# Kernel optimization log

Hardware: AMD Instinct MI355X
Metric: run time of the kernel (lower is better)

The kernel has to match this reference:

```python
import jax, jax.numpy as jnp
import numpy as np

N_NODES = 50000
N_EDGES = 800000
IN_CH, HID, OUT_CH = 3, 64, 768
NEG_SLOPE = 0.01  # torch LeakyReLU default
BN_EPS = 1e-5


def _gcn_conv(x, edge_index, W, b):
    # PyG GCNConv: add self-loops, symmetric degree normalization, scatter-add.
    n = x.shape[0]
    loops = jnp.arange(n, dtype=edge_index.dtype)
    src = jnp.concatenate([edge_index[0], loops])
    dst = jnp.concatenate([edge_index[1], loops])
    deg = jax.ops.segment_sum(jnp.ones(src.shape[0], x.dtype), dst, num_segments=n)
    dinv = jnp.where(deg > 0, jax.lax.rsqrt(deg), 0.0)
    norm = dinv[src] * dinv[dst]                      # [E+N]
    h = x @ W                                          # [N, out]
    msg = h[src] * norm[:, None]                       # gather + edge scale
    return jax.ops.segment_sum(msg, dst, num_segments=n) + b


def _block(x, edge_index, W, b, gamma, beta):
    h = _gcn_conv(x, edge_index, W, b)
    h = jnp.where(h >= 0, h, NEG_SLOPE * h)            # LeakyReLU
    mean = h.mean(axis=0)
    var = h.var(axis=0)                                # biased, as torch BN train
    h = (h - mean) * jax.lax.rsqrt(var + BN_EPS) * gamma + beta
    return h                                           # dropout: identity (eval)


def _glorot(key, fan_in, fan_out):
    s = np.sqrt(6.0 / (fan_in + fan_out)).astype(np.float32)
    return jax.random.uniform(key, (fan_in, fan_out), jnp.float32, -s, s)


def setup_inputs() -> dict:
    key = jax.random.key(0)
    ks = jax.random.split(key, 8)
    x = jax.random.normal(ks[0], (N_NODES, IN_CH), jnp.float32)
    edge_index = jax.random.randint(ks[1], (2, N_EDGES), 0, N_NODES, jnp.int64)
    inp = {"x": x, "edge_index": edge_index}
    inp["W1"] = _glorot(ks[2], IN_CH, HID)
    inp["b1"] = jnp.zeros((HID,), jnp.float32)
    inp["g1"] = jnp.ones((HID,), jnp.float32)
    inp["be1"] = jnp.zeros((HID,), jnp.float32)
    inp["W2"] = _glorot(ks[3], HID, HID)
    inp["b2"] = jnp.zeros((HID,), jnp.float32)
    inp["g2"] = jnp.ones((HID,), jnp.float32)
    inp["be2"] = jnp.zeros((HID,), jnp.float32)
    inp["W3"] = _glorot(ks[4], HID, HID)
    inp["b3"] = jnp.zeros((HID,), jnp.float32)
    inp["g3"] = jnp.ones((HID,), jnp.float32)
    inp["be3"] = jnp.zeros((HID,), jnp.float32)
    inp["Wmu"] = _glorot(ks[5], HID, OUT_CH)
    inp["bmu"] = jnp.zeros((OUT_CH,), jnp.float32)
    inp["Wls"] = _glorot(ks[6], HID, OUT_CH)
    inp["bls"] = jnp.zeros((OUT_CH,), jnp.float32)
    return inp


def reference(x, edge_index, W1, b1, g1, be1, W2, b2, g2, be2, W3, b3, g3, be3, Wmu, bmu, Wls, bls):
    h = _block(x, edge_index, W1, b1, g1, be1)
    h = _block(h, edge_index, W2, b2, g2, be2)
    h = _block(h, edge_index, W3, b3, g3, be3)
    mu = _gcn_conv(h, edge_index, Wmu, bmu)
    logstd = _gcn_conv(h, edge_index, Wls, bls)
    return (mu, logstd)
```

## Files before the change

kernel.cpp:

```cpp
#include <hip/hip_runtime.h>
#include <cstddef>


#define NEG_SLOPE 0.01f
#define BN_EPS 1e-5f

__global__ __launch_bounds__(256) void init_k(int* __restrict__ cnt,
                                              float* __restrict__ bns, int N) {
  int i = blockIdx.x * 256 + threadIdx.x;
  if (i < N) cnt[i] = 0;
  if (i < 384) bns[i] = 0.0f;
}

__global__ __launch_bounds__(256) void hist_k(const int* __restrict__ dst,
                                              int* __restrict__ cnt, int E) {
  int e = blockIdx.x * 256 + threadIdx.x;
  if (e < E) atomicAdd(&cnt[dst[e]], 1);
}

__global__ __launch_bounds__(1024) void scanA(const int* __restrict__ cnt,
                                              int* __restrict__ pre,
                                              int* __restrict__ bsum, int N) {
  __shared__ int sh[1024];
  const int t = threadIdx.x;
  const int i = blockIdx.x * 1024 + t;
  int c = (i < N) ? cnt[i] : 0;
  sh[t] = c;
  __syncthreads();
  for (int off = 1; off < 1024; off <<= 1) {
    int v = (t >= off) ? sh[t - off] : 0;
    __syncthreads();
    sh[t] += v;
    __syncthreads();
  }
  if (i < N) pre[i] = sh[t] - c;
  if (t == 1023) bsum[blockIdx.x] = sh[t];
}

__global__ __launch_bounds__(64) void scanB(int* __restrict__ bsum, int nb) {
  int t = threadIdx.x;
  int orig = (t < nb) ? bsum[t] : 0;
  int v = orig;
#pragma unroll
  for (int off = 1; off < 64; off <<= 1) {
    int u = __shfl_up(v, off);
    if (t >= off) v += u;
  }
  if (t < nb) bsum[t] = v - orig;
}

__global__ __launch_bounds__(256) void scanC(const int* __restrict__ cnt,
                                             int* __restrict__ rowptr,
                                             int* __restrict__ cursor,
                                             const int* __restrict__ bsum,
                                             float* __restrict__ dinv,
                                             int N, int E) {
  int i = blockIdx.x * 256 + threadIdx.x;
  if (i < N) {
    int rp = rowptr[i] + bsum[i >> 10];
    rowptr[i] = rp;
    cursor[i] = rp;
    dinv[i] = rsqrtf((float)(cnt[i] + 1));
  }
  if (i == 0) rowptr[N] = E;
}

__global__ __launch_bounds__(256) void fill_k(const int* __restrict__ src,
                                              const int* __restrict__ dst,
                                              int* __restrict__ cursor,
                                              int* __restrict__ eidx, int E) {
  int e = blockIdx.x * 256 + threadIdx.x;
  if (e >= E) return;
  int p = atomicAdd(&cursor[dst[e]], 1);
  eidx[p] = src[e];
}

__global__ __launch_bounds__(256) void l1_fused(
    const int* __restrict__ rowptr, const int* __restrict__ eidx,
    const float* __restrict__ x, const float* __restrict__ dinv,
    const float* __restrict__ W1, const float* __restrict__ b1,
    float* __restrict__ Z, float* __restrict__ q, float* __restrict__ bns, int N) {
  const int t = threadIdx.x, lane = t & 63, wid = t >> 6;
  const int gw = blockIdx.x * 4 + wid;
  const int nw = gridDim.x * 4;
  const float w0 = W1[lane], w1 = W1[64 + lane], w2 = W1[128 + lane];
  const float bb = b1[lane];
  float s1 = 0.f, s2 = 0.f;
  for (int node = gw; node < N; node += nw) {
    int beg = rowptr[node], end = rowptr[node + 1];
    float a0 = 0.f, a1 = 0.f, a2 = 0.f, aq = 0.f;
    for (int e = beg + lane; e < end; e += 64) {
      int s = eidx[e];
      float dv = dinv[s];
      a0 += x[s * 3] * dv;
      a1 += x[s * 3 + 1] * dv;
      a2 += x[s * 3 + 2] * dv;
      aq += dv;
    }
#pragma unroll
    for (int off = 32; off; off >>= 1) {
      a0 += __shfl_xor(a0, off);
      a1 += __shfl_xor(a1, off);
      a2 += __shfl_xor(a2, off);
      aq += __shfl_xor(aq, off);
    }
    float dv = dinv[node];
    a0 += x[node * 3] * dv;
    a1 += x[node * 3 + 1] * dv;
    a2 += x[node * 3 + 2] * dv;
    aq += dv;
    float u = dv * (a0 * w0 + a1 * w1 + a2 * w2) + bb;
    float o = u >= 0.f ? u : NEG_SLOPE * u;
    Z[(size_t)node * 64 + lane] = o * dv;
    s1 += o;
    s2 += o * o;
    if (lane == 0) q[node] = aq;
  }
  __shared__ float red[8][64];
  red[wid][lane] = s1;
  red[4 + wid][lane] = s2;
  __syncthreads();
  if (t < 64) {
    atomicAdd(&bns[t], red[0][t] + red[1][t] + red[2][t] + red[3][t]);
    atomicAdd(&bns[64 + t], red[4][t] + red[5][t] + red[6][t] + red[7][t]);
  }
}

__global__ __launch_bounds__(256) void gather64(const int* __restrict__ rowptr,
                                                const int* __restrict__ eidx,
                                                const float* __restrict__ Z,
                                                float* __restrict__ G, int N) {
  int node = blockIdx.x * 4 + (threadIdx.x >> 6);
  if (node >= N) return;
  int lane = threadIdx.x & 63;
  int slot = lane >> 4;
  int c4 = (lane & 15) << 2;
  int beg = rowptr[node], end = rowptr[node + 1];
  float ax = 0.f, ay = 0.f, az = 0.f, aw = 0.f;
  int e = beg + slot;
  for (; e + 4 < end; e += 8) {
    int s0 = eidx[e], s1 = eidx[e + 4];
    float4 v0 = *(const float4*)(Z + (size_t)s0 * 64 + c4);
    float4 v1 = *(const float4*)(Z + (size_t)s1 * 64 + c4);
    ax += v0.x + v1.x;
    ay += v0.y + v1.y;
    az += v0.z + v1.z;
    aw += v0.w + v1.w;
  }
  if (e < end) {
    int s0 = eidx[e];
    float4 v0 = *(const float4*)(Z + (size_t)s0 * 64 + c4);
    ax += v0.x; ay += v0.y; az += v0.z; aw += v0.w;
  }
#pragma unroll
  for (int off = 16; off < 64; off <<= 1) {
    ax += __shfl_xor(ax, off);
    ay += __shfl_xor(ay, off);
    az += __shfl_xor(az, off);
    aw += __shfl_xor(aw, off);
  }
  if (slot == 0) {
    float4 self = *(const float4*)(Z + (size_t)node * 64 + c4);
    float4 o = make_float4(ax + self.x, ay + self.y, az + self.z, aw + self.w);
    *(float4*)(G + (size_t)node * 64 + c4) = o;
  }
}

__global__ __launch_bounds__(256) void prep_small(
    const float* __restrict__ bns, const float* __restrict__ g,
    const float* __restrict__ be, const float* __restrict__ W,
    float* __restrict__ Wc, float* __restrict__ cx, float invN) {
  __shared__ float sc[64], sh[64], part[4][64];
  int t = threadIdx.x;
  if (t < 64) {
    float mean = bns[t] * invN;
    float var = bns[64 + t] * invN - mean * mean;
    float s = g[t] * rsqrtf(var + BN_EPS);
    sc[t] = s;
    sh[t] = be[t] - mean * s;
  }
  __syncthreads();
  int c = t & 63, kq = t >> 6;
  float p = 0.f;
  for (int k = kq * 16; k < kq * 16 + 16; ++k) {
    float w = W[k * 64 + c];
    Wc[k * 64 + c] = sc[k] * w;
    p += sh[k] * w;
  }
  part[kq][c] = p;
  __syncthreads();
  if (t < 64) cx[t] = part[0][t] + part[1][t] + part[2][t] + part[3][t];
}

__global__ __launch_bounds__(256) void prep_head(
    const float* __restrict__ bns, const float* __restrict__ g,
    const float* __restrict__ be, const float* __restrict__ Wmu,
    const float* __restrict__ Wls, float* __restrict__ Wmc,
    float* __restrict__ Wlc, float* __restrict__ cmu, float* __restrict__ cls,
    float invN) {
  __shared__ float sc[64], sh[64], part[2][128];
  int t = threadIdx.x;
  if (t < 64) {
    float mean = bns[t] * invN;
    float var = bns[64 + t] * invN - mean * mean;
    float s = g[t] * rsqrtf(var + BN_EPS);
    sc[t] = s;
    sh[t] = be[t] - mean * s;
  }
  __syncthreads();
  int blk = blockIdx.x;
  int head = blk >= 6 ? 1 : 0;
  int c0 = (head ? blk - 6 : blk) * 128;
  const float* W = head ? Wls : Wmu;
  float* Wc = head ? Wlc : Wmc;
  float* cx = head ? cls : cmu;
  int c = c0 + (t & 127), kh = t >> 7;
  float p = 0.f;
  for (int k = kh * 32; k < kh * 32 + 32; ++k) {
    float w = W[(size_t)k * 768 + c];
    Wc[(size_t)k * 768 + c] = sc[k] * w;
    p += sh[k] * w;
  }
  part[kh][t & 127] = p;
  __syncthreads();
  if (t < 128) cx[c0 + t] = part[0][t] + part[1][t];
}

__global__ __launch_bounds__(256, 4) void gemm_bnq(
    const float* __restrict__ G, const float* __restrict__ dinv,
    const float* __restrict__ q, const float* __restrict__ Wc,
    const float* __restrict__ cx, const float* __restrict__ b,
    float* __restrict__ Z, float* __restrict__ bns, int N) {
  __shared__ __align__(16) float P[64][68];
  __shared__ __align__(16) float Ws[64][64];
  const int t = threadIdx.x;
  const int r0 = blockIdx.x * 64;

  for (int i = t; i < 1024; i += 256) {
    int r = i >> 4, k4 = (i & 15) << 2, gr = r0 + r;
    float4 v = make_float4(0.f, 0.f, 0.f, 0.f);
    if (gr < N) v = *(const float4*)(G + (size_t)gr * 64 + k4);
    *(float4*)&P[r][k4] = v;
  }
  for (int i = t; i < 4096; i += 256) Ws[i >> 6][i & 63] = Wc[i];
  __syncthreads();

  const int tr = t >> 4, tc4 = (t & 15) << 2;
  float acc[4][4] = {};
#pragma unroll 8
  for (int k = 0; k < 64; ++k) {
    float4 w = *(const float4*)&Ws[k][tc4];
#pragma unroll
    for (int i = 0; i < 4; ++i) {
      float a = P[tr + 16 * i][k];
      acc[i][0] += a * w.x;
      acc[i][1] += a * w.y;
      acc[i][2] += a * w.z;
      acc[i][3] += a * w.w;
    }
  }

  float s1[4] = {0.f, 0.f, 0.f, 0.f}, s2[4] = {0.f, 0.f, 0.f, 0.f};
  float4 bb = *(const float4*)(b + tc4);
  float4 cc = *(const float4*)(cx + tc4);
#pragma unroll
  for (int i = 0; i < 4; ++i) {
    int r = r0 + tr + 16 * i;
    if (r < N) {
      float dv = dinv[r];
      float dq = dv * q[r];
      float u0 = acc[i][0] * dv + dq * cc.x + bb.x;
      float u1 = acc[i][1] * dv + dq * cc.y + bb.y;
      float u2 = acc[i][2] * dv + dq * cc.z + bb.z;
      float u3 = acc[i][3] * dv + dq * cc.w + bb.w;
      float o0 = u0 >= 0.f ? u0 : NEG_SLOPE * u0;
      float o1 = u1 >= 0.f ? u1 : NEG_SLOPE * u1;
      float o2 = u2 >= 0.f ? u2 : NEG_SLOPE * u2;
      float o3 = u3 >= 0.f ? u3 : NEG_SLOPE * u3;
      float4 z = make_float4(o0 * dv, o1 * dv, o2 * dv, o3 * dv);
      *(float4*)(Z + (size_t)r * 64 + tc4) = z;
      s1[0] += o0; s2[0] += o0 * o0;
      s1[1] += o1; s2[1] += o1 * o1;
      s1[2] += o2; s2[2] += o2 * o2;
      s1[3] += o3; s2[3] += o3 * o3;
    }
  }
  __syncthreads();
  float (*red1)[64] = (float(*)[64]) & Ws[0][0];
  float (*red2)[64] = (float(*)[64]) & Ws[16][0];
#pragma unroll
  for (int j = 0; j < 4; ++j) {
    red1[tr][tc4 + j] = s1[j];
    red2[tr][tc4 + j] = s2[j];
  }
  __syncthreads();
  if (t < 64) {
    float a1 = 0.f, a2 = 0.f;
#pragma unroll
    for (int i = 0; i < 16; ++i) {
      a1 += red1[i][t];
      a2 += red2[i][t];
    }
    atomicAdd(&bns[t], a1);
    atomicAdd(&bns[64 + t], a2);
  }
}

__global__ __launch_bounds__(256, 3) void head_gemm3(
    const float* __restrict__ G, const float* __restrict__ dinv,
    const float* __restrict__ q, const float* __restrict__ Wmc,
    const float* __restrict__ cmu, const float* __restrict__ bmu,
    const float* __restrict__ Wlc, const float* __restrict__ cls,
    const float* __restrict__ bls, float* __restrict__ OUT, int N) {
  __shared__ __align__(16) float P[128][68];
  __shared__ __align__(16) float Ws[32][128];
  const int t = threadIdx.x;
  const int r0 = blockIdx.x * 128;
  const int yy = blockIdx.y;
  const int head = (yy >= 6) ? 1 : 0;
  const int c0 = (head ? yy - 6 : yy) * 128;
  const float* W = head ? Wlc : Wmc;
  const float* cx = head ? cls : cmu;
  const float* b = head ? bls : bmu;
  float* O = OUT + (head ? (size_t)N * 768 : 0);

  for (int i = t; i < 2048; i += 256) {
    int r = i >> 4, k4 = (i & 15) << 2, gr = r0 + r;
    float4 v = make_float4(0.f, 0.f, 0.f, 0.f);
    if (gr < N) v = *(const float4*)(G + (size_t)gr * 64 + k4);
    *(float4*)&P[r][k4] = v;
  }

  const int tr = t >> 4;
  const int tc = t & 15;
  float acc[8][8] = {};

  for (int kk = 0; kk < 64; kk += 32) {
    __syncthreads();
    for (int i = t; i < 1024; i += 256) {
      int k = i >> 5, c4 = (i & 31) << 2;
      *(float4*)&Ws[k][c4] = *(const float4*)(W + (size_t)(kk + k) * 768 + c0 + c4);
    }
    __syncthreads();
#pragma unroll 2
    for (int k = 0; k < 32; ++k) {
      float4 w0 = *(const float4*)&Ws[k][tc * 4];
      float4 w1 = *(const float4*)&Ws[k][64 + tc * 4];
#pragma unroll
      for (int i = 0; i < 8; ++i) {
        float a = P[tr + 16 * i][kk + k];
        acc[i][0] += a * w0.x;
        acc[i][1] += a * w0.y;
        acc[i][2] += a * w0.z;
        acc[i][3] += a * w0.w;
        acc[i][4] += a * w1.x;
        acc[i][5] += a * w1.y;
        acc[i][6] += a * w1.z;
        acc[i][7] += a * w1.w;
      }
    }
  }

  float4 bb0 = *(const float4*)(b + c0 + tc * 4);
  float4 bb1 = *(const float4*)(b + c0 + 64 + tc * 4);
  float4 cc0 = *(const float4*)(cx + c0 + tc * 4);
  float4 cc1 = *(const float4*)(cx + c0 + 64 + tc * 4);
#pragma unroll
  for (int i = 0; i < 8; ++i) {
    int r = r0 + tr + 16 * i;
    if (r < N) {
      float dv = dinv[r];
      float dq = dv * q[r];
      float4 o0 = make_float4(acc[i][0] * dv + dq * cc0.x + bb0.x,
                              acc[i][1] * dv + dq * cc0.y + bb0.y,
                              acc[i][2] * dv + dq * cc0.z + bb0.z,
                              acc[i][3] * dv + dq * cc0.w + bb0.w);
      float4 o1 = make_float4(acc[i][4] * dv + dq * cc1.x + bb1.x,
                              acc[i][5] * dv + dq * cc1.y + bb1.y,
                              acc[i][6] * dv + dq * cc1.z + bb1.z,
                              acc[i][7] * dv + dq * cc1.w + bb1.w);
      *(float4*)(O + (size_t)r * 768 + c0 + tc * 4) = o0;
      *(float4*)(O + (size_t)r * 768 + c0 + 64 + tc * 4) = o1;
    }
  }
}

extern "C" void kernel_launch(void* const* d_in, const int* in_sizes, int n_in,
                              void* d_out, int out_size, void* d_ws, size_t ws_size,
                              hipStream_t stream) {
  const float* x   = (const float*)d_in[0];
  const int*   ei  = (const int*)d_in[1];
  const float* W1  = (const float*)d_in[2];
  const float* b1  = (const float*)d_in[3];
  const float* g1  = (const float*)d_in[4];
  const float* be1 = (const float*)d_in[5];
  const float* W2  = (const float*)d_in[6];
  const float* b2  = (const float*)d_in[7];
  const float* g2  = (const float*)d_in[8];
  const float* be2 = (const float*)d_in[9];
  const float* W3  = (const float*)d_in[10];
  const float* b3  = (const float*)d_in[11];
  const float* g3  = (const float*)d_in[12];
  const float* be3 = (const float*)d_in[13];
  const float* Wmu = (const float*)d_in[14];
  const float* bmu = (const float*)d_in[15];
  const float* Wls = (const float*)d_in[16];
  const float* bls = (const float*)d_in[17];

  const int N = in_sizes[0] / 3;
  const int E = in_sizes[1] / 2;
  const int* src = ei;
  const int* dst = ei + E;
  float* out = (float*)d_out;

  char* ws = (char*)d_ws;
  size_t o = 0;
  float* dinv = (float*)(ws + o); o += (size_t)N * 4;
  float* qv   = (float*)(ws + o); o += (size_t)N * 4;
  float* bns  = (float*)(ws + o); o += 384 * 4;
  float* W2c  = (float*)(ws + o); o += 4096 * 4;
  float* c2   = (float*)(ws + o); o += 64 * 4;
  float* W3c  = (float*)(ws + o); o += 4096 * 4;
  float* c3   = (float*)(ws + o); o += 64 * 4;
  float* Wmc  = (float*)(ws + o); o += (size_t)64 * 768 * 4;
  float* cmu  = (float*)(ws + o); o += 768 * 4;
  float* Wlc  = (float*)(ws + o); o += (size_t)64 * 768 * 4;
  float* cls  = (float*)(ws + o); o += 768 * 4;
  int* cnt    = (int*)(ws + o);   o += (size_t)N * 4;
  int* rowptr = (int*)(ws + o);   o += ((size_t)N + 1) * 4;
  int* cursor = (int*)(ws + o);   o += (size_t)N * 4;
  int* bsum   = (int*)(ws + o);   o += 64 * 4;
  int* eidx   = (int*)(ws + o);   o += (size_t)E * 4;
  float* B0   = (float*)(ws + o); o += (size_t)N * 64 * 4;
  float* B1   = (float*)(ws + o); o += (size_t)N * 64 * 4;

  const float invN = 1.0f / (float)N;
  int nbN = (N + 255) / 256;
  int nbE = (E + 255) / 256;
  int gb  = (N + 63) / 64;
  int gb2 = (N + 127) / 128;
  int wb  = (N + 3) / 4;
  int sbA = (N + 1023) / 1024;

  init_k<<<nbN, 256, 0, stream>>>(cnt, bns, N);
  hist_k<<<nbE, 256, 0, stream>>>(dst, cnt, E);
  scanA<<<sbA, 1024, 0, stream>>>(cnt, rowptr, bsum, N);
  scanB<<<1, 64, 0, stream>>>(bsum, sbA);
  scanC<<<nbN, 256, 0, stream>>>(cnt, rowptr, cursor, bsum, dinv, N, E);
  fill_k<<<nbE, 256, 0, stream>>>(src, dst, cursor, eidx, E);

  l1_fused<<<1024, 256, 0, stream>>>(rowptr, eidx, x, dinv, W1, b1, B0, qv, bns, N);
  prep_small<<<1, 256, 0, stream>>>(bns + 0, g1, be1, W2, W2c, c2, invN);

  gather64<<<wb, 256, 0, stream>>>(rowptr, eidx, B0, B1, N);
  gemm_bnq<<<gb, 256, 0, stream>>>(B1, dinv, qv, W2c, c2, b2, B0, bns + 128, N);
  prep_small<<<1, 256, 0, stream>>>(bns + 128, g2, be2, W3, W3c, c3, invN);

  gather64<<<wb, 256, 0, stream>>>(rowptr, eidx, B0, B1, N);
  gemm_bnq<<<gb, 256, 0, stream>>>(B1, dinv, qv, W3c, c3, b3, B0, bns + 256, N);
  prep_head<<<12, 256, 0, stream>>>(bns + 256, g3, be3, Wmu, Wls, Wmc, Wlc, cmu, cls, invN);

  gather64<<<wb, 256, 0, stream>>>(rowptr, eidx, B0, B1, N);
  dim3 hgrid(gb2, 12);
  head_gemm3<<<hgrid, 256, 0, stream>>>(B1, dinv, qv, Wmc, cmu, bmu, Wlc, cls, bls, out, N);
}
```

Baseline: 440.9 us.

## Compute head GEMM with split-bf16 MFMA instead of FP32 FMA

```diff
diff --git a/kernel.cpp b/kernel.cpp
--- a/kernel.cpp
+++ b/kernel.cpp
@@ -4,6 +4,15 @@
 
 #define NEG_SLOPE 0.01f
 #define BN_EPS 1e-5f
+
+typedef unsigned short u16;
+typedef __attribute__((ext_vector_type(8))) short bf16x8;
+typedef __attribute__((ext_vector_type(4))) float f32x4;
+
+__device__ __forceinline__ unsigned bf16_rne(float x) {
+  unsigned u = __float_as_uint(x);
+  return (u + 0x7fffu + ((u >> 16) & 1u)) >> 16;
+}
 
 __global__ __launch_bounds__(256) void init_k(int* __restrict__ cnt,
                                               float* __restrict__ bns, int N) {
@@ -166,6 +175,55 @@
   }
 }
 
+__global__ __launch_bounds__(256) void gather64h(const int* __restrict__ rowptr,
+                                                 const int* __restrict__ eidx,
+                                                 const float* __restrict__ Z,
+                                                 u16* __restrict__ Ghi,
+                                                 u16* __restrict__ Glo, int N) {
+  int node = blockIdx.x * 4 + (threadIdx.x >> 6);
+  if (node >= N) return;
+  int lane = threadIdx.x & 63;
+  int slot = lane >> 4;
+  int c4 = (lane & 15) << 2;
+  int beg = rowptr[node], end = rowptr[node + 1];
+  float ax = 0.f, ay = 0.f, az = 0.f, aw = 0.f;
+  int e = beg + slot;
+  for (; e + 4 < end; e += 8) {
+    int s0 = eidx[e], s1 = eidx[e + 4];
+    float4 v0 = *(const float4*)(Z + (size_t)s0 * 64 + c4);
+    float4 v1 = *(const float4*)(Z + (size_t)s1 * 64 + c4);
+    ax += v0.x + v1.x;
+    ay += v0.y + v1.y;
+    az += v0.z + v1.z;
+    aw += v0.w + v1.w;
+  }
+  if (e < end) {
+    int s0 = eidx[e];
+    float4 v0 = *(const float4*)(Z + (size_t)s0 * 64 + c4);
+    ax += v0.x; ay += v0.y; az += v0.z; aw += v0.w;
+  }
+#pragma unroll
+  for (int off = 16; off < 64; off <<= 1) {
+    ax += __shfl_xor(ax, off);
+    ay += __shfl_xor(ay, off);
+    az += __shfl_xor(az, off);
+    aw += __shfl_xor(aw, off);
+  }
+  if (slot == 0) {
+    float4 self = *(const float4*)(Z + (size_t)node * 64 + c4);
+    float o0 = ax + self.x, o1 = ay + self.y, o2 = az + self.z, o3 = aw + self.w;
+    unsigned h0 = bf16_rne(o0), h1 = bf16_rne(o1), h2 = bf16_rne(o2), h3 = bf16_rne(o3);
+    unsigned l0 = bf16_rne(o0 - __uint_as_float(h0 << 16));
+    unsigned l1 = bf16_rne(o1 - __uint_as_float(h1 << 16));
+    unsigned l2 = bf16_rne(o2 - __uint_as_float(h2 << 16));
+    unsigned l3 = bf16_rne(o3 - __uint_as_float(h3 << 16));
+    uint2 hv = make_uint2(h0 | (h1 << 16), h2 | (h3 << 16));
+    uint2 lv = make_uint2(l0 | (l1 << 16), l2 | (l3 << 16));
+    *(uint2*)(Ghi + (size_t)node * 64 + c4) = hv;
+    *(uint2*)(Glo + (size_t)node * 64 + c4) = lv;
+  }
+}
+
 __global__ __launch_bounds__(256) void prep_small(
     const float* __restrict__ bns, const float* __restrict__ g,
     const float* __restrict__ be, const float* __restrict__ W,
@@ -195,9 +253,8 @@
 __global__ __launch_bounds__(256) void prep_head(
     const float* __restrict__ bns, const float* __restrict__ g,
     const float* __restrict__ be, const float* __restrict__ Wmu,
-    const float* __restrict__ Wls, float* __restrict__ Wmc,
-    float* __restrict__ Wlc, float* __restrict__ cmu, float* __restrict__ cls,
-    float invN) {
+    const float* __restrict__ Wls, u16* __restrict__ Bh, u16* __restrict__ Bl,
+    float* __restrict__ cmu, float* __restrict__ cls, float invN) {
   __shared__ float sc[64], sh[64], part[2][128];
   int t = threadIdx.x;
   if (t < 64) {
@@ -210,18 +267,27 @@
   __syncthreads();
   int blk = blockIdx.x;
   int head = blk >= 6 ? 1 : 0;
-  int c0 = (head ? blk - 6 : blk) * 128;
+  int cc = head ? blk - 6 : blk;
+  int c0 = cc * 128;
   const float* W = head ? Wls : Wmu;
-  float* Wc = head ? Wlc : Wmc;
   float* cx = head ? cls : cmu;
-  int c = c0 + (t & 127), kh = t >> 7;
+  int cl = t & 127, kh = t >> 7;
+  int c = c0 + cl;
+  int ct = cl >> 4, jc = cl & 15;
+  size_t base = (size_t)(head * 6 + cc) * 2 * 8 * 64 * 8;
   float p = 0.f;
   for (int k = kh * 32; k < kh * 32 + 32; ++k) {
     float w = W[(size_t)k * 768 + c];
-    Wc[(size_t)k * 768 + c] = sc[k] * w;
+    float wc = sc[k] * w;
     p += sh[k] * w;
-  }
-  part[kh][t & 127] = p;
+    unsigned hi = bf16_rne(wc);
+    unsigned lo = bf16_rne(wc - __uint_as_float(hi << 16));
+    int lane = ((k >> 3) & 3) * 16 + jc;
+    size_t idx = base + (((size_t)kh * 8 + ct) * 64 + lane) * 8 + (k & 7);
+    Bh[idx] = (u16)hi;
+    Bl[idx] = (u16)lo;
+  }
+  part[kh][cl] = p;
   __syncthreads();
   if (t < 128) cx[c0 + t] = part[0][t] + part[1][t];
 }
@@ -306,81 +372,73 @@
   }
 }
 
-__global__ __launch_bounds__(256, 3) void head_gemm3(
-    const float* __restrict__ G, const float* __restrict__ dinv,
-    const float* __restrict__ q, const float* __restrict__ Wmc,
+__global__ __launch_bounds__(256) void head_mfma(
+    const u16* __restrict__ Ghi, const u16* __restrict__ Glo,
+    const float* __restrict__ dinv, const float* __restrict__ q,
+    const u16* __restrict__ Bh, const u16* __restrict__ Bl,
     const float* __restrict__ cmu, const float* __restrict__ bmu,
-    const float* __restrict__ Wlc, const float* __restrict__ cls,
-    const float* __restrict__ bls, float* __restrict__ OUT, int N) {
-  __shared__ __align__(16) float P[128][68];
-  __shared__ __align__(16) float Ws[32][128];
+    const float* __restrict__ cls, const float* __restrict__ bls,
+    float* __restrict__ OUT, int N) {
   const int t = threadIdx.x;
-  const int r0 = blockIdx.x * 128;
+  const int w = t >> 6, l = t & 63;
+  const int r0 = blockIdx.x * 64 + w * 16;
   const int yy = blockIdx.y;
   const int head = (yy >= 6) ? 1 : 0;
-  const int c0 = (head ? yy - 6 : yy) * 128;
-  const float* W = head ? Wlc : Wmc;
+  const int cc = head ? yy - 6 : yy;
+  const int c0 = cc * 128;
   const float* cx = head ? cls : cmu;
-  const float* b = head ? bls : bmu;
+  const float* bb = head ? bls : bmu;
   float* O = OUT + (head ? (size_t)N * 768 : 0);
 
-  for (int i = t; i < 2048; i += 256) {
-    int r = i >> 4, k4 = (i & 15) << 2, gr = r0 + r;
-    float4 v = make_float4(0.f, 0.f, 0.f, 0.f);
-    if (gr < N) v = *(const float4*)(G + (size_t)gr * 64 + k4);
-    *(float4*)&P[r][k4] = v;
-  }
-
-  const int tr = t >> 4;
-  const int tc = t & 15;
-  float acc[8][8] = {};
-
-  for (int kk = 0; kk < 64; kk += 32) {
-    __syncthreads();
-    for (int i = t; i < 1024; i += 256) {
-      int k = i >> 5, c4 = (i & 31) << 2;
-      *(float4*)&Ws[k][c4] = *(const float4*)(W + (size_t)(kk + k) * 768 + c0 + c4);
-    }
-    __syncthreads();
-#pragma unroll 2
-    for (int k = 0; k < 32; ++k) {
-      float4 w0 = *(const float4*)&Ws[k][tc * 4];
-      float4 w1 = *(const float4*)&Ws[k][64 + tc * 4];
-#pragma unroll
-      for (int i = 0; i < 8; ++i) {
-        float a = P[tr + 16 * i][kk + k];
-        acc[i][0] += a * w0.x;
-        acc[i][1] += a * w0.y;
-        acc[i][2] += a * w0.z;
-        acc[i][3] += a * w0.w;
-        acc[i][4] += a * w1.x;
-        acc[i][5] += a * w1.y;
-        acc[i][6] += a * w1.z;
-        acc[i][7] += a * w1.w;
-      }
-    }
-  }
-
-  float4 bb0 = *(const float4*)(b + c0 + tc * 4);
-  float4 bb1 = *(const float4*)(b + c0 + 64 + tc * 4);
-  float4 cc0 = *(const float4*)(cx + c0 + tc * 4);
-  float4 cc1 = *(const float4*)(cx + c0 + 64 + tc * 4);
-#pragma unroll
-  for (int i = 0; i < 8; ++i) {
-    int r = r0 + tr + 16 * i;
-    if (r < N) {
-      float dv = dinv[r];
-      float dq = dv * q[r];
-      float4 o0 = make_float4(acc[i][0] * dv + dq * cc0.x + bb0.x,
-                              acc[i][1] * dv + dq * cc0.y + bb0.y,
-                              acc[i][2] * dv + dq * cc0.z + bb0.z,
-                              acc[i][3] * dv + dq * cc0.w + bb0.w);
-      float4 o1 = make_float4(acc[i][4] * dv + dq * cc1.x + bb1.x,
-                              acc[i][5] * dv + dq * cc1.y + bb1.y,
-                              acc[i][6] * dv + dq * cc1.z + bb1.z,
-                              acc[i][7] * dv + dq * cc1.w + bb1.w);
-      *(float4*)(O + (size_t)r * 768 + c0 + tc * 4) = o0;
-      *(float4*)(O + (size_t)r * 768 + c0 + 64 + tc * 4) = o1;
+  int arow = r0 + (l & 15);
+  if (arow >= N) arow = N - 1;
+  const u16* gh = Ghi + (size_t)arow * 64 + ((l >> 4) << 3);
+  const u16* gl = Glo + (size_t)arow * 64 + ((l >> 4) << 3);
+  const bf16x8 ah0 = *(const bf16x8*)gh;
+  const bf16x8 ah1 = *(const bf16x8*)(gh + 32);
+  const bf16x8 al0 = *(const bf16x8*)gl;
+  const bf16x8 al1 = *(const bf16x8*)(gl + 32);
+
+  const size_t base = (size_t)(head * 6 + cc) * 2 * 8 * 64 * 8;
+  const u16* bhp = Bh + base;
+  const u16* blp = Bl + base;
+
+  f32x4 acc[8];
+#pragma unroll
+  for (int ct = 0; ct < 8; ++ct) {
+    const bf16x8 bh0 = *(const bf16x8*)(bhp + (((size_t)ct) * 64 + l) * 8);
+    const bf16x8 bh1 = *(const bf16x8*)(bhp + (((size_t)(8 + ct)) * 64 + l) * 8);
+    const bf16x8 bl0 = *(const bf16x8*)(blp + (((size_t)ct) * 64 + l) * 8);
+    const bf16x8 bl1 = *(const bf16x8*)(blp + (((size_t)(8 + ct)) * 64 + l) * 8);
+    f32x4 a = {0.f, 0.f, 0.f, 0.f};
+    a = __builtin_amdgcn_mfma_f32_16x16x32_bf16(ah0, bh0, a, 0, 0, 0);
+    a = __builtin_amdgcn_mfma_f32_16x16x32_bf16(ah1, bh1, a, 0, 0, 0);
+    a = __builtin_amdgcn_mfma_f32_16x16x32_bf16(ah0, bl0, a, 0, 0, 0);
+    a = __builtin_amdgcn_mfma_f32_16x16x32_bf16(ah1, bl1, a, 0, 0, 0);
+    a = __builtin_amdgcn_mfma_f32_16x16x32_bf16(al0, bh0, a, 0, 0, 0);
+    a = __builtin_amdgcn_mfma_f32_16x16x32_bf16(al1, bh1, a, 0, 0, 0);
+    acc[ct] = a;
+  }
+
+  const int jc = l & 15;
+  const int rbase = r0 + ((l >> 4) << 2);
+  float dv[4], dq[4];
+#pragma unroll
+  for (int r = 0; r < 4; ++r) {
+    int row = rbase + r;
+    int rc = row < N ? row : N - 1;
+    dv[r] = dinv[rc];
+    dq[r] = dv[r] * q[rc];
+  }
+#pragma unroll
+  for (int ct = 0; ct < 8; ++ct) {
+    int col = c0 + ct * 16 + jc;
+    float cxv = cx[col], bbv = bb[col];
+#pragma unroll
+    for (int r = 0; r < 4; ++r) {
+      int row = rbase + r;
+      if (row < N)
+        O[(size_t)row * 768 + col] = acc[ct][r] * dv[r] + dq[r] * cxv + bbv;
     }
   }
 }
@@ -422,10 +480,12 @@
   float* c2   = (float*)(ws + o); o += 64 * 4;
   float* W3c  = (float*)(ws + o); o += 4096 * 4;
   float* c3   = (float*)(ws + o); o += 64 * 4;
-  float* Wmc  = (float*)(ws + o); o += (size_t)64 * 768 * 4;
+  u16* Bh     = (u16*)(ws + o);   o += (size_t)12 * 2 * 8 * 64 * 8 * 2;
+  u16* Bl     = (u16*)(ws + o);   o += (size_t)12 * 2 * 8 * 64 * 8 * 2;
   float* cmu  = (float*)(ws + o); o += 768 * 4;
-  float* Wlc  = (float*)(ws + o); o += (size_t)64 * 768 * 4;
   float* cls  = (float*)(ws + o); o += 768 * 4;
+  u16* Ghi    = (u16*)(ws + o);   o += (size_t)N * 64 * 2;
+  u16* Glo    = (u16*)(ws + o);   o += (size_t)N * 64 * 2;
   int* cnt    = (int*)(ws + o);   o += (size_t)N * 4;
   int* rowptr = (int*)(ws + o);   o += ((size_t)N + 1) * 4;
   int* cursor = (int*)(ws + o);   o += (size_t)N * 4;
@@ -438,7 +498,6 @@
   int nbN = (N + 255) / 256;
   int nbE = (E + 255) / 256;
   int gb  = (N + 63) / 64;
-  int gb2 = (N + 127) / 128;
   int wb  = (N + 3) / 4;
   int sbA = (N + 1023) / 1024;
 
@@ -458,9 +517,10 @@
 
   gather64<<<wb, 256, 0, stream>>>(rowptr, eidx, B0, B1, N);
   gemm_bnq<<<gb, 256, 0, stream>>>(B1, dinv, qv, W3c, c3, b3, B0, bns + 256, N);
-  prep_head<<<12, 256, 0, stream>>>(bns + 256, g3, be3, Wmu, Wls, Wmc, Wlc, cmu, cls, invN);
-
-  gather64<<<wb, 256, 0, stream>>>(rowptr, eidx, B0, B1, N);
-  dim3 hgrid(gb2, 12);
-  head_gemm3<<<hgrid, 256, 0, stream>>>(B1, dinv, qv, Wmc, cmu, bmu, Wlc, cls, bls, out, N);
-}
+  prep_head<<<12, 256, 0, stream>>>(bns + 256, g3, be3, Wmu, Wls, Bh, Bl, cmu, cls, invN);
+
+  gather64h<<<wb, 256, 0, stream>>>(rowptr, eidx, B0, Ghi, Glo, N);
+  dim3 hgrid(gb, 12);
+  head_mfma<<<hgrid, 256, 0, stream>>>(Ghi, Glo, dinv, qv, Bh, Bl,
+                                       cmu, bmu, cls, bls, out, N);
+}
```

New measurement: 427.6 us. 1.03x faster.
